# Kernel optimization log

Measured on AMD Instinct MI355X. Metric: run time of the kernel, lower is better.

Reference implementation:

```python
import jax, jax.numpy as jnp
import numpy as np

D_MODEL = 1024
N_HEADS = 16
HEAD_DIM = D_MODEL // N_HEADS
SPARSITY = 0.5  # torch.rand(...) < sparsity_factor -> True means masked (disallowed)


def setup_inputs() -> dict:
    key = jax.random.key(0)
    ks = jax.random.split(key, 12)
    B, S, D = 2, 2048, D_MODEL
    query = jax.random.normal(ks[0], (B, S, D), dtype=jnp.float32)
    key_t = jax.random.normal(ks[1], (B, S, D), dtype=jnp.float32)
    value = jax.random.normal(ks[2], (B, S, D), dtype=jnp.float32)
    # per-forward random boolean mask, materialized deterministically here
    mask = jax.random.uniform(ks[3], (B, S, S)) < SPARSITY
    scale = 1.0 / np.sqrt(D)
    Wq = jax.random.uniform(ks[4], (D, D), jnp.float32, -scale, scale)
    Wk = jax.random.uniform(ks[5], (D, D), jnp.float32, -scale, scale)
    Wv = jax.random.uniform(ks[6], (D, D), jnp.float32, -scale, scale)
    Wo = jax.random.uniform(ks[7], (D, D), jnp.float32, -scale, scale)
    bq = jnp.zeros((D,), jnp.float32)
    bk = jnp.zeros((D,), jnp.float32)
    bv = jnp.zeros((D,), jnp.float32)
    bo = jnp.zeros((D,), jnp.float32)
    return {"query": query, "key": key_t, "value": value, "mask": mask,
            "Wq": Wq, "Wk": Wk, "Wv": Wv, "Wo": Wo,
            "bq": bq, "bk": bk, "bv": bv, "bo": bo}


def reference(query, key, value, mask, Wq, Wk, Wv, Wo, bq, bk, bv, bo):
    B, S, D = query.shape
    H, hd = N_HEADS, HEAD_DIM
    # in-projections (torch uses x @ W.T + b)
    q = (query @ Wq.T + bq).reshape(B, S, H, hd).transpose(0, 2, 1, 3)  # (B,H,S,hd)
    k = (key @ Wk.T + bk).reshape(B, S, H, hd).transpose(0, 2, 1, 3)
    v = (value @ Wv.T + bv).reshape(B, S, H, hd).transpose(0, 2, 1, 3)
    scores = jnp.einsum('bhqd,bhkd->bhqk', q, k) / jnp.sqrt(jnp.float32(hd))
    # bool mask: True = disallowed; broadcast over heads
    scores = jnp.where(mask[:, None, :, :], -jnp.inf, scores)
    attn = jax.nn.softmax(scores, axis=-1)  # dropout inactive at eval
    out = jnp.einsum('bhqk,bhkd->bhqd', attn, v)  # (B,H,S,hd)
    out = out.transpose(0, 2, 1, 3).reshape(B, S, D)
    return out @ Wo.T + bo
```

## Files before the change

### kernel.cpp

```cpp
#include <hip/hip_runtime.h>
#include <stdint.h>

#define MTOK   4096
#define DMODEL 1024
#define SEQ    2048
#define NH     16
#define HD     64
#define LDK    72
#define LDP    72
#define QSCL   0.18033688f
#define NWORDS (2 * SEQ * SEQ / 64)

typedef _Float16 h8  __attribute__((ext_vector_type(8)));
typedef _Float16 h4  __attribute__((ext_vector_type(4)));
typedef _Float16 h2  __attribute__((ext_vector_type(2)));
typedef __fp16   fp16x2 __attribute__((ext_vector_type(2)));
typedef float    f16v __attribute__((ext_vector_type(16)));
typedef float    f4  __attribute__((ext_vector_type(4)));

typedef __attribute__((address_space(1))) const unsigned int g_u32;
typedef __attribute__((address_space(3))) unsigned int       l_u32;

__device__ __forceinline__ void g2l16(const void* g, void* l) {
    __builtin_amdgcn_global_load_lds((g_u32*)(unsigned long long)g,
                                     (l_u32*)(unsigned int)(unsigned long long)l,
                                     16, 0, 0);
}

__device__ __forceinline__ h2 pkrtz(float a, float b) {
    fp16x2 r = __builtin_amdgcn_cvt_pkrtz(a, b);
    return __builtin_bit_cast(h2, r);
}

#if __has_builtin(__builtin_amdgcn_exp2f)
#define E2(x) __builtin_amdgcn_exp2f(x)
#else
#define E2(x) exp2f(x)
#endif

__global__ __launch_bounds__(256) void prep_kernel(
    const float* __restrict__ s0, const float* __restrict__ s1,
    const float* __restrict__ s2, const float* __restrict__ s3,
    const float* __restrict__ s4, const float* __restrict__ s5,
    const float* __restrict__ s6,
    _Float16* __restrict__ d0, _Float16* __restrict__ d1,
    _Float16* __restrict__ d2, _Float16* __restrict__ d3,
    _Float16* __restrict__ d4, _Float16* __restrict__ d5,
    _Float16* __restrict__ d6,
    const unsigned char* __restrict__ mb, const unsigned int* __restrict__ mu,
    unsigned long long* __restrict__ mout) {
    const int z = blockIdx.y;
    const int gid = blockIdx.x * 256 + threadIdx.x;
    const int stride = gridDim.x * 256;
    if (z < 7) {
        const float* s = (z == 0) ? s0 : (z == 1) ? s1 : (z == 2) ? s2
                       : (z == 3) ? s3 : (z == 4) ? s4 : (z == 5) ? s5 : s6;
        _Float16* d = (z == 0) ? d0 : (z == 1) ? d1 : (z == 2) ? d2
                    : (z == 3) ? d3 : (z == 4) ? d4 : (z == 5) ? d5 : d6;
        const int n4 = (z < 3) ? (MTOK * DMODEL / 4) : (DMODEL * DMODEL / 4);
        for (int i = gid; i < n4; i += stride) {
            float4 v = ((const float4*)s)[i];
            h4 o = {(_Float16)v.x, (_Float16)v.y, (_Float16)v.z, (_Float16)v.w};
            ((h4*)d)[i] = o;
        }
    } else {
        __shared__ int wsum[4];
        int cnt = 0;
        const uchar4* mp4 = (const uchar4*)mb;
#pragma unroll
        for (int i = 0; i < 8; ++i) {
            uchar4 v = mp4[threadIdx.x * 8 + i];
            cnt += (v.x != 0) + (v.y != 0) + (v.z != 0) + (v.w != 0);
        }
#pragma unroll
        for (int off = 32; off > 0; off >>= 1) cnt += __shfl_down(cnt, off, 64);
        if ((threadIdx.x & 63) == 0) wsum[threadIdx.x >> 6] = cnt;
        __syncthreads();
        const int byteflag = (wsum[0] + wsum[1] + wsum[2] + wsum[3]) > 2500;

        for (int w = gid; w < NWORDS; w += stride) {
            unsigned long long bits = 0ull;
            if (byteflag) {
                const uint4* p = (const uint4*)(mb + (size_t)w * 64);
#pragma unroll
                for (int i = 0; i < 4; ++i) {
                    uint4 v = p[i];
                    unsigned dw[4] = {v.x, v.y, v.z, v.w};
#pragma unroll
                    for (int j = 0; j < 4; ++j) {
                        unsigned d = dw[j];
                        unsigned nib = (unsigned)((d & 0xFFu) != 0)
                                     | ((unsigned)((d & 0xFF00u) != 0) << 1)
                                     | ((unsigned)((d & 0xFF0000u) != 0) << 2)
                                     | ((unsigned)((d >> 24) != 0) << 3);
                        bits |= (unsigned long long)nib << (i * 16 + j * 4);
                    }
                }
            } else {
                const uint4* p = (const uint4*)(mu + (size_t)w * 64);
#pragma unroll
                for (int i = 0; i < 16; ++i) {
                    uint4 v = p[i];
                    unsigned nib = (unsigned)(v.x != 0u)
                                 | ((unsigned)(v.y != 0u) << 1)
                                 | ((unsigned)(v.z != 0u) << 2)
                                 | ((unsigned)(v.w != 0u) << 3);
                    bits |= (unsigned long long)nib << (i * 4);
                }
            }
            mout[w] = bits;
        }
    }
}

template <int MODE, int BM, int BN>
__device__ __forceinline__ void gemm16_body(const _Float16* __restrict__ A,
                                            const _Float16* __restrict__ W,
                                            const float* __restrict__ bias,
                                            void* __restrict__ outv,
                                            float scale) {
    __shared__ __align__(16) _Float16 Asb[BM * 64];
    __shared__ __align__(16) _Float16 Bsb[BN * 64];
    constexpr int NI = BM / 32, NJ = BN / 32;
    constexpr int WM = BM / 2,  WN = BN / 2;
    constexpr int RA = BM * 128 / 4096;
    constexpr int RB = BN * 128 / 4096;
    const int tid = threadIdx.x;
    const int wv = tid >> 6, lane = tid & 63;
    const int l15 = lane & 15, g = lane >> 4;
    const int wy = wv >> 1, wx = wv & 1;
    const int m0 = blockIdx.x * BM, n0 = blockIdx.y * BN;

    f4 acc[NI][NJ];
#pragma unroll
    for (int i = 0; i < NI; ++i)
#pragma unroll
        for (int j = 0; j < NJ; ++j) acc[i][j] = (f4){0.f, 0.f, 0.f, 0.f};

    const char* Ab = (const char*)A;
    const char* Wb = (const char*)W;
    int srowA[RA], scolA[RA];
#pragma unroll
    for (int r = 0; r < RA; ++r) {
        const int o = (r * 256 + tid) * 16;
        srowA[r] = o >> 7;
        scolA[r] = (((o >> 4) & 7) ^ (srowA[r] & 7)) * 16;
    }
    int srowB[RB], scolB[RB];
#pragma unroll
    for (int r = 0; r < RB; ++r) {
        const int o = (r * 256 + tid) * 16;
        srowB[r] = o >> 7;
        scolB[r] = (((o >> 4) & 7) ^ (srowB[r] & 7)) * 16;
    }

    for (int kt = 0; kt < 16; ++kt) {
        const int k0b = kt * 128;
        __syncthreads();
#pragma unroll
        for (int r = 0; r < RA; ++r)
            g2l16(Ab + (size_t)(m0 + srowA[r]) * 2048 + k0b + scolA[r],
                  (char*)Asb + (r * 256 + tid) * 16);
#pragma unroll
        for (int r = 0; r < RB; ++r)
            g2l16(Wb + (size_t)(n0 + srowB[r]) * 2048 + k0b + scolB[r],
                  (char*)Bsb + (r * 256 + tid) * 16);
        __syncthreads();

#pragma unroll
        for (int ksub = 0; ksub < 2; ++ksub) {
            h8 af[NI], bf[NJ];
#pragma unroll
            for (int t = 0; t < NI; ++t) {
                const int row = wy * WM + t * 16 + l15;
                const int pos = (ksub * 4 + g) ^ (row & 7);
                af[t] = *(const h8*)(Asb + row * 64 + pos * 8);
            }
#pragma unroll
            for (int t = 0; t < NJ; ++t) {
                const int row = wx * WN + t * 16 + l15;
                const int pos = (ksub * 4 + g) ^ (row & 7);
                bf[t] = *(const h8*)(Bsb + row * 64 + pos * 8);
            }
#pragma unroll
            for (int i = 0; i < NI; ++i)
#pragma unroll
                for (int j = 0; j < NJ; ++j) {
                    if (MODE == 2)
                        acc[i][j] = __builtin_amdgcn_mfma_f32_16x16x32_f16(
                            bf[j], af[i], acc[i][j], 0, 0, 0);
                    else
                        acc[i][j] = __builtin_amdgcn_mfma_f32_16x16x32_f16(
                            af[i], bf[j], acc[i][j], 0, 0, 0);
                }
        }
    }

#pragma unroll
    for (int j = 0; j < NJ; ++j) {
#pragma unroll
        for (int i = 0; i < NI; ++i) {
            if (MODE == 2) {
                const int m = m0 + wy * WM + i * 16 + l15;
                const int b = m >> 11, s = m & 2047;
#pragma unroll
                for (int r = 0; r < 4; ++r) {
                    const int n = n0 + wx * WN + j * 16 + g * 4 + r;
                    const int h = n >> 6, d = n & 63;
                    ((_Float16*)outv)[(((size_t)(b * NH + h)) * HD + d) * SEQ + s] =
                        (_Float16)(acc[i][j][r] + bias[n]);
                }
            } else {
                const int n = n0 + wx * WN + j * 16 + l15;
                const float bb = bias[n];
                const int mbase = m0 + wy * WM + i * 16 + g * 4;
                if (MODE == 1) {
                    const int h = n >> 6, d = n & 63;
#pragma unroll
                    for (int r = 0; r < 4; ++r) {
                        const int m = mbase + r;
                        const int b = m >> 11, s = m & 2047;
                        ((_Float16*)outv)[(((size_t)(b * NH + h)) * SEQ + s) * HD + d] =
                            (_Float16)((acc[i][j][r] + bb) * scale);
                    }
                } else {
#pragma unroll
                    for (int r = 0; r < 4; ++r)
                        ((float*)outv)[(size_t)(mbase + r) * DMODEL + n] =
                            acc[i][j][r] + bb;
                }
            }
        }
    }
}

__global__ __launch_bounds__(256) void qkv_gemm16_kernel(
    const _Float16* __restrict__ xq, const _Float16* __restrict__ xk,
    const _Float16* __restrict__ xv,
    const _Float16* __restrict__ Wq, const _Float16* __restrict__ Wk,
    const _Float16* __restrict__ Wv,
    const float* __restrict__ bq, const float* __restrict__ bk,
    const float* __restrict__ bv,
    _Float16* __restrict__ q_out, _Float16* __restrict__ k_out,
    _Float16* __restrict__ vt_out) {
    const int z = blockIdx.z;
    if (z == 0)      gemm16_body<1, 128, 128>(xq, Wq, bq, (void*)q_out, QSCL);
    else if (z == 1) gemm16_body<1, 128, 128>(xk, Wk, bk, (void*)k_out, 1.0f);
    else             gemm16_body<2, 128, 128>(xv, Wv, bv, (void*)vt_out, 1.0f);
}

__global__ __launch_bounds__(256) void out_gemm16_kernel(
    const _Float16* __restrict__ X, const _Float16* __restrict__ W,
    const float* __restrict__ bias, float* __restrict__ out) {
    gemm16_body<0, 64, 128>(X, W, bias, (void*)out, 1.0f);
}

__global__ __launch_bounds__(256) void attn_kernel(
    const _Float16* __restrict__ Q, const _Float16* __restrict__ K,
    const _Float16* __restrict__ Vt,
    const unsigned long long* __restrict__ mbits,
    _Float16* __restrict__ out) {
    __shared__ __align__(16) _Float16 Ks[2][64 * LDK];
    __shared__ __align__(16) _Float16 Vs[2][64 * LDK];
    __shared__ __align__(16) _Float16 Ps[128 * LDP];

    const int tid = threadIdx.x;
    const int wv = tid >> 6, lane = tid & 63;
    const int l31 = lane & 31, hi = lane >> 5;
    const int q0 = blockIdx.x * 128;
    const int bh = blockIdx.y;
    const int b = bh >> 4, h = bh & 15;
    const size_t bho = (size_t)bh * (SEQ * HD);
    const int qrow = q0 + wv * 32 + l31;

    h8 qf[4];
    const _Float16* qp = Q + bho + (size_t)qrow * HD;
#pragma unroll
    for (int ks = 0; ks < 4; ++ks) qf[ks] = *(const h8*)(qp + ks * 16 + hi * 8);

    f16v Ot[2];
#pragma unroll
    for (int mt = 0; mt < 2; ++mt)
#pragma unroll
        for (int r = 0; r < 16; ++r) Ot[mt][r] = 0.f;
    float l_r = 0.f;

    const int sr = tid >> 2;
    const int scol = (tid & 3) * 16;
    const _Float16* kg = K + bho;
    const _Float16* vg = Vt + bho;
    _Float16* prow = &Ps[(wv * 32 + l31) * LDP];
    const unsigned long long* mrow =
        mbits + ((size_t)b * SEQ + qrow) * (SEQ / 64);

    h8 kr0 = *(const h8*)(kg + (size_t)sr * HD + scol);
    h8 kr1 = *(const h8*)(kg + (size_t)sr * HD + scol + 8);
    h8 vr0 = *(const h8*)(vg + (size_t)sr * SEQ + scol);
    h8 vr1 = *(const h8*)(vg + (size_t)sr * SEQ + scol + 8);
    uint2 mw = *(const uint2*)(mrow);
    *(h8*)(&Ks[0][sr * LDK + scol])     = kr0;
    *(h8*)(&Ks[0][sr * LDK + scol + 8]) = kr1;
    *(h8*)(&Vs[0][sr * LDK + scol])     = vr0;
    *(h8*)(&Vs[0][sr * LDK + scol + 8]) = vr1;
    __syncthreads();

    for (int kt = 0; kt < 32; ++kt) {
        const int cur = kt & 1;
        uint2 mw_n;
        if (kt < 31) {
            const int k0n = (kt + 1) * 64;
            kr0 = *(const h8*)(kg + (size_t)(k0n + sr) * HD + scol);
            kr1 = *(const h8*)(kg + (size_t)(k0n + sr) * HD + scol + 8);
            vr0 = *(const h8*)(vg + (size_t)sr * SEQ + k0n + scol);
            vr1 = *(const h8*)(vg + (size_t)sr * SEQ + k0n + scol + 8);
            mw_n = *(const uint2*)(mrow + kt + 1);
        }

        f16v sc0, sc1;
#pragma unroll
        for (int r = 0; r < 16; ++r) { sc0[r] = 0.f; sc1[r] = 0.f; }
#pragma unroll
        for (int ks = 0; ks < 4; ++ks) {
            h8 kf0 = *(const h8*)(&Ks[cur][l31 * LDK + ks * 16 + hi * 8]);
            h8 kf1 = *(const h8*)(&Ks[cur][(32 + l31) * LDK + ks * 16 + hi * 8]);
            sc0 = __builtin_amdgcn_mfma_f32_32x32x16_f16(kf0, qf[ks], sc0, 0, 0, 0);
            sc1 = __builtin_amdgcn_mfma_f32_32x32x16_f16(kf1, qf[ks], sc1, 0, 0, 0);
        }

        float ps = 0.f;
#pragma unroll
        for (int mt = 0; mt < 2; ++mt) {
            const unsigned w = mt ? mw.y : mw.x;
            const f16v& s = mt ? sc1 : sc0;
#pragma unroll
            for (int g4 = 0; g4 < 4; ++g4) {
                const int sh = g4 * 8 + hi * 4;
                float p0 = E2(((w >> (sh + 0)) & 1u) ? -1e30f : s[g4 * 4 + 0]);
                float p1 = E2(((w >> (sh + 1)) & 1u) ? -1e30f : s[g4 * 4 + 1]);
                float p2 = E2(((w >> (sh + 2)) & 1u) ? -1e30f : s[g4 * 4 + 2]);
                float p3 = E2(((w >> (sh + 3)) & 1u) ? -1e30f : s[g4 * 4 + 3]);
                h2 lo  = pkrtz(p0, p1);
                h2 hi2 = pkrtz(p2, p3);
                ps += p0 + p1 + p2 + p3;
                h4 ph = {lo.x, lo.y, hi2.x, hi2.y};
                *(h4*)(prow + mt * 32 + g4 * 8 + hi * 4) = ph;
            }
        }
        l_r += ps;

        h8 pf[4];
#pragma unroll
        for (int ks = 0; ks < 4; ++ks)
            pf[ks] = *(const h8*)(prow + ks * 16 + hi * 8);
#pragma unroll
        for (int ks = 0; ks < 4; ++ks) {
            h8 vf0 = *(const h8*)(&Vs[cur][l31 * LDK + ks * 16 + hi * 8]);
            h8 vf1 = *(const h8*)(&Vs[cur][(32 + l31) * LDK + ks * 16 + hi * 8]);
            Ot[0] = __builtin_amdgcn_mfma_f32_32x32x16_f16(vf0, pf[ks], Ot[0], 0, 0, 0);
            Ot[1] = __builtin_amdgcn_mfma_f32_32x32x16_f16(vf1, pf[ks], Ot[1], 0, 0, 0);
        }

        if (kt < 31) {
            const int nxt = cur ^ 1;
            *(h8*)(&Ks[nxt][sr * LDK + scol])     = kr0;
            *(h8*)(&Ks[nxt][sr * LDK + scol + 8]) = kr1;
            *(h8*)(&Vs[nxt][sr * LDK + scol])     = vr0;
            *(h8*)(&Vs[nxt][sr * LDK + scol + 8]) = vr1;
            mw = mw_n;
        }
        __syncthreads();
    }

    l_r += __shfl_xor(l_r, 32);
    const float inv = 1.0f / l_r;
    _Float16* op = out + ((size_t)b * SEQ + qrow) * DMODEL + h * HD;
#pragma unroll
    for (int mt = 0; mt < 2; ++mt)
#pragma unroll
        for (int g4 = 0; g4 < 4; ++g4) {
            const int d = mt * 32 + g4 * 8 + hi * 4;
            h4 ov = {(_Float16)(Ot[mt][g4 * 4 + 0] * inv),
                     (_Float16)(Ot[mt][g4 * 4 + 1] * inv),
                     (_Float16)(Ot[mt][g4 * 4 + 2] * inv),
                     (_Float16)(Ot[mt][g4 * 4 + 3] * inv)};
            *(h4*)(op + d) = ov;
        }
}

extern "C" void kernel_launch(void* const* d_in, const int* in_sizes, int n_in,
                              void* d_out, int out_size, void* d_ws, size_t ws_size,
                              hipStream_t stream) {
    const float* query = (const float*)d_in[0];
    const float* key_  = (const float*)d_in[1];
    const float* value = (const float*)d_in[2];
    const void*  mask  = d_in[3];
    const float* Wq = (const float*)d_in[4];
    const float* Wk = (const float*)d_in[5];
    const float* Wv = (const float*)d_in[6];
    const float* Wo = (const float*)d_in[7];
    const float* bq = (const float*)d_in[8];
    const float* bk = (const float*)d_in[9];
    const float* bv = (const float*)d_in[10];
    const float* bo = (const float*)d_in[11];

    char* ws = (char*)d_ws;
    _Float16* xq  = (_Float16*)(ws + 256);
    _Float16* xk  = xq + (size_t)MTOK * DMODEL;
    _Float16* xv  = xk + (size_t)MTOK * DMODEL;
    _Float16* Wqh = xv + (size_t)MTOK * DMODEL;
    _Float16* Wkh = Wqh + (size_t)DMODEL * DMODEL;
    _Float16* Wvh = Wkh + (size_t)DMODEL * DMODEL;
    _Float16* Woh = Wvh + (size_t)DMODEL * DMODEL;
    _Float16* q_ws  = Woh + (size_t)DMODEL * DMODEL;
    _Float16* k_ws  = q_ws + (size_t)MTOK * DMODEL;
    _Float16* vt_ws = k_ws + (size_t)MTOK * DMODEL;
    _Float16* a_ws  = vt_ws + (size_t)MTOK * DMODEL;
    unsigned long long* mb_ws =
        (unsigned long long*)(a_ws + (size_t)MTOK * DMODEL);

    prep_kernel<<<dim3(1024, 8), 256, 0, stream>>>(
        query, key_, value, Wq, Wk, Wv, Wo, xq, xk, xv, Wqh, Wkh, Wvh, Woh,
        (const unsigned char*)mask, (const unsigned int*)mask, mb_ws);

    dim3 gqkv(MTOK / 128, DMODEL / 128, 3);
    qkv_gemm16_kernel<<<gqkv, 256, 0, stream>>>(xq, xk, xv, Wqh, Wkh, Wvh,
                                                bq, bk, bv, q_ws, k_ws, vt_ws);

    dim3 gattn(SEQ / 128, 2 * NH);
    attn_kernel<<<gattn, 256, 0, stream>>>(q_ws, k_ws, vt_ws, mb_ws, a_ws);

    dim3 gout(MTOK / 64, DMODEL / 128);
    out_gemm16_kernel<<<gout, 256, 0, stream>>>(a_ws, Woh, bo, (float*)d_out);
}
```

Measured before the change: 276.0 us.

## Split attention KV loop across two wave groups and keep P in registers

The attention kernel now uses 512 threads, and two groups of four waves each process alternate 64-key tiles for the same 128 queries. Their partial outputs and row sums are merged through shared memory at the end. The P matrix no longer goes through an LDS round-trip: v_permlane32_swap rearranges the packed fp16 probabilities in registers into MFMA operand layout, and row sums are taken with fdot2 on the rounded values. s_setprio is raised around the MFMA blocks. This buys more parallelism per CU and less LDS traffic, at the cost of a final merge step and more LDS per block.

```diff
diff --git a/kernel.cpp b/kernel.cpp
--- a/kernel.cpp
+++ b/kernel.cpp
@@ -7,7 +7,6 @@
 #define NH     16
 #define HD     64
 #define LDK    72
-#define LDP    72
 #define QSCL   0.18033688f
 #define NWORDS (2 * SEQ * SEQ / 64)
 
@@ -17,6 +16,7 @@
 typedef __fp16   fp16x2 __attribute__((ext_vector_type(2)));
 typedef float    f16v __attribute__((ext_vector_type(16)));
 typedef float    f4  __attribute__((ext_vector_type(4)));
+typedef int      iv4 __attribute__((ext_vector_type(4)));
 
 typedef __attribute__((address_space(1))) const unsigned int g_u32;
 typedef __attribute__((address_space(3))) unsigned int       l_u32;
@@ -37,6 +37,16 @@
 #else
 #define E2(x) exp2f(x)
 #endif
+
+__device__ __forceinline__ float dot2sum(int v, float acc) {
+    h2 a = __builtin_bit_cast(h2, v);
+#if __has_builtin(__builtin_amdgcn_fdot2)
+    h2 one2 = {(_Float16)1.0f, (_Float16)1.0f};
+    return __builtin_amdgcn_fdot2(a, one2, acc, false);
+#else
+    return acc + (float)a.x + (float)a.y;
+#endif
+}
 
 __global__ __launch_bounds__(256) void prep_kernel(
     const float* __restrict__ s0, const float* __restrict__ s1,
@@ -255,23 +265,23 @@
     gemm16_body<0, 64, 128>(X, W, bias, (void*)out, 1.0f);
 }
 
-__global__ __launch_bounds__(256) void attn_kernel(
+__global__ __launch_bounds__(512, 4) void attn_kernel(
     const _Float16* __restrict__ Q, const _Float16* __restrict__ K,
     const _Float16* __restrict__ Vt,
     const unsigned long long* __restrict__ mbits,
     _Float16* __restrict__ out) {
-    __shared__ __align__(16) _Float16 Ks[2][64 * LDK];
-    __shared__ __align__(16) _Float16 Vs[2][64 * LDK];
-    __shared__ __align__(16) _Float16 Ps[128 * LDP];
+    __shared__ __align__(16) _Float16 Ks[2][2][64 * LDK];
+    __shared__ __align__(16) _Float16 Vs[2][2][64 * LDK];
 
     const int tid = threadIdx.x;
     const int wv = tid >> 6, lane = tid & 63;
+    const int grp = wv >> 2, wvg = wv & 3;
     const int l31 = lane & 31, hi = lane >> 5;
     const int q0 = blockIdx.x * 128;
     const int bh = blockIdx.y;
     const int b = bh >> 4, h = bh & 15;
     const size_t bho = (size_t)bh * (SEQ * HD);
-    const int qrow = q0 + wv * 32 + l31;
+    const int qrow = q0 + wvg * 32 + l31;
 
     h8 qf[4];
     const _Float16* qp = Q + bho + (size_t)qrow * HD;
@@ -285,106 +295,136 @@
         for (int r = 0; r < 16; ++r) Ot[mt][r] = 0.f;
     float l_r = 0.f;
 
-    const int sr = tid >> 2;
-    const int scol = (tid & 3) * 16;
+    const int gtid = tid & 255;
+    const int sr = gtid >> 2;
+    const int scol = (gtid & 3) * 16;
     const _Float16* kg = K + bho;
     const _Float16* vg = Vt + bho;
-    _Float16* prow = &Ps[(wv * 32 + l31) * LDP];
     const unsigned long long* mrow =
         mbits + ((size_t)b * SEQ + qrow) * (SEQ / 64);
 
-    h8 kr0 = *(const h8*)(kg + (size_t)sr * HD + scol);
-    h8 kr1 = *(const h8*)(kg + (size_t)sr * HD + scol + 8);
-    h8 vr0 = *(const h8*)(vg + (size_t)sr * SEQ + scol);
-    h8 vr1 = *(const h8*)(vg + (size_t)sr * SEQ + scol + 8);
-    uint2 mw = *(const uint2*)(mrow);
-    *(h8*)(&Ks[0][sr * LDK + scol])     = kr0;
-    *(h8*)(&Ks[0][sr * LDK + scol + 8]) = kr1;
-    *(h8*)(&Vs[0][sr * LDK + scol])     = vr0;
-    *(h8*)(&Vs[0][sr * LDK + scol + 8]) = vr1;
+    {
+        const int k0 = grp * 64;
+        h8 a0 = *(const h8*)(kg + (size_t)(k0 + sr) * HD + scol);
+        h8 a1 = *(const h8*)(kg + (size_t)(k0 + sr) * HD + scol + 8);
+        h8 a2 = *(const h8*)(vg + (size_t)sr * SEQ + k0 + scol);
+        h8 a3 = *(const h8*)(vg + (size_t)sr * SEQ + k0 + scol + 8);
+        *(h8*)(&Ks[grp][0][sr * LDK + scol])     = a0;
+        *(h8*)(&Ks[grp][0][sr * LDK + scol + 8]) = a1;
+        *(h8*)(&Vs[grp][0][sr * LDK + scol])     = a2;
+        *(h8*)(&Vs[grp][0][sr * LDK + scol + 8]) = a3;
+    }
+    uint2 mw = *(const uint2*)(mrow + grp);
     __syncthreads();
 
-    for (int kt = 0; kt < 32; ++kt) {
-        const int cur = kt & 1;
+    for (int it = 0; it < 16; ++it) {
+        const int cur = it & 1;
+        const int kt = 2 * it + grp;
+        h8 kr0, kr1, vr0, vr1;
         uint2 mw_n;
-        if (kt < 31) {
-            const int k0n = (kt + 1) * 64;
+        if (it < 15) {
+            const int k0n = (kt + 2) * 64;
             kr0 = *(const h8*)(kg + (size_t)(k0n + sr) * HD + scol);
             kr1 = *(const h8*)(kg + (size_t)(k0n + sr) * HD + scol + 8);
             vr0 = *(const h8*)(vg + (size_t)sr * SEQ + k0n + scol);
             vr1 = *(const h8*)(vg + (size_t)sr * SEQ + k0n + scol + 8);
-            mw_n = *(const uint2*)(mrow + kt + 1);
+            mw_n = *(const uint2*)(mrow + kt + 2);
         }
 
         f16v sc0, sc1;
 #pragma unroll
         for (int r = 0; r < 16; ++r) { sc0[r] = 0.f; sc1[r] = 0.f; }
+        __builtin_amdgcn_s_setprio(1);
 #pragma unroll
         for (int ks = 0; ks < 4; ++ks) {
-            h8 kf0 = *(const h8*)(&Ks[cur][l31 * LDK + ks * 16 + hi * 8]);
-            h8 kf1 = *(const h8*)(&Ks[cur][(32 + l31) * LDK + ks * 16 + hi * 8]);
+            h8 kf0 = *(const h8*)(&Ks[grp][cur][l31 * LDK + ks * 16 + hi * 8]);
+            h8 kf1 = *(const h8*)(&Ks[grp][cur][(32 + l31) * LDK + ks * 16 + hi * 8]);
             sc0 = __builtin_amdgcn_mfma_f32_32x32x16_f16(kf0, qf[ks], sc0, 0, 0, 0);
             sc1 = __builtin_amdgcn_mfma_f32_32x32x16_f16(kf1, qf[ks], sc1, 0, 0, 0);
         }
-
-        float ps = 0.f;
+        __builtin_amdgcn_s_setprio(0);
+
+        int rp[8][2];
 #pragma unroll
         for (int mt = 0; mt < 2; ++mt) {
             const unsigned w = mt ? mw.y : mw.x;
+            const unsigned wl = w >> (hi * 4);
             const f16v& s = mt ? sc1 : sc0;
 #pragma unroll
             for (int g4 = 0; g4 < 4; ++g4) {
-                const int sh = g4 * 8 + hi * 4;
-                float p0 = E2(((w >> (sh + 0)) & 1u) ? -1e30f : s[g4 * 4 + 0]);
-                float p1 = E2(((w >> (sh + 1)) & 1u) ? -1e30f : s[g4 * 4 + 1]);
-                float p2 = E2(((w >> (sh + 2)) & 1u) ? -1e30f : s[g4 * 4 + 2]);
-                float p3 = E2(((w >> (sh + 3)) & 1u) ? -1e30f : s[g4 * 4 + 3]);
-                h2 lo  = pkrtz(p0, p1);
-                h2 hi2 = pkrtz(p2, p3);
-                ps += p0 + p1 + p2 + p3;
-                h4 ph = {lo.x, lo.y, hi2.x, hi2.y};
-                *(h4*)(prow + mt * 32 + g4 * 8 + hi * 4) = ph;
-            }
-        }
-        l_r += ps;
-
-        h8 pf[4];
-#pragma unroll
-        for (int ks = 0; ks < 4; ++ks)
-            pf[ks] = *(const h8*)(prow + ks * 16 + hi * 8);
+                float p0 = E2(((wl >> (g4 * 8 + 0)) & 1u) ? -1e30f : s[g4 * 4 + 0]);
+                float p1 = E2(((wl >> (g4 * 8 + 1)) & 1u) ? -1e30f : s[g4 * 4 + 1]);
+                float p2 = E2(((wl >> (g4 * 8 + 2)) & 1u) ? -1e30f : s[g4 * 4 + 2]);
+                float p3 = E2(((wl >> (g4 * 8 + 3)) & 1u) ? -1e30f : s[g4 * 4 + 3]);
+                rp[mt * 4 + g4][0] = __builtin_bit_cast(int, pkrtz(p0, p1));
+                rp[mt * 4 + g4][1] = __builtin_bit_cast(int, pkrtz(p2, p3));
+            }
+        }
+
+        float l0 = 0.f, l1 = 0.f;
 #pragma unroll
         for (int ks = 0; ks < 4; ++ks) {
-            h8 vf0 = *(const h8*)(&Vs[cur][l31 * LDK + ks * 16 + hi * 8]);
-            h8 vf1 = *(const h8*)(&Vs[cur][(32 + l31) * LDK + ks * 16 + hi * 8]);
-            Ot[0] = __builtin_amdgcn_mfma_f32_32x32x16_f16(vf0, pf[ks], Ot[0], 0, 0, 0);
-            Ot[1] = __builtin_amdgcn_mfma_f32_32x32x16_f16(vf1, pf[ks], Ot[1], 0, 0, 0);
-        }
-
-        if (kt < 31) {
+            int a0 = rp[2 * ks][0], a1 = rp[2 * ks][1];
+            int b0 = rp[2 * ks + 1][0], b1 = rp[2 * ks + 1][1];
+            asm volatile("v_permlane32_swap_b32 %0, %1" : "+v"(a0), "+v"(b0));
+            asm volatile("v_permlane32_swap_b32 %0, %1" : "+v"(a1), "+v"(b1));
+            l0 = dot2sum(a0, l0); l1 = dot2sum(a1, l1);
+            l0 = dot2sum(b0, l0); l1 = dot2sum(b1, l1);
+            iv4 pi = {a0, a1, b0, b1};
+            h8 pf = __builtin_bit_cast(h8, pi);
+            __builtin_amdgcn_s_setprio(1);
+            h8 vf0 = *(const h8*)(&Vs[grp][cur][l31 * LDK + ks * 16 + hi * 8]);
+            h8 vf1 = *(const h8*)(&Vs[grp][cur][(32 + l31) * LDK + ks * 16 + hi * 8]);
+            Ot[0] = __builtin_amdgcn_mfma_f32_32x32x16_f16(vf0, pf, Ot[0], 0, 0, 0);
+            Ot[1] = __builtin_amdgcn_mfma_f32_32x32x16_f16(vf1, pf, Ot[1], 0, 0, 0);
+            __builtin_amdgcn_s_setprio(0);
+        }
+        l_r += l0 + l1;
+
+        if (it < 15) {
             const int nxt = cur ^ 1;
-            *(h8*)(&Ks[nxt][sr * LDK + scol])     = kr0;
-            *(h8*)(&Ks[nxt][sr * LDK + scol + 8]) = kr1;
-            *(h8*)(&Vs[nxt][sr * LDK + scol])     = vr0;
-            *(h8*)(&Vs[nxt][sr * LDK + scol + 8]) = vr1;
+            *(h8*)(&Ks[grp][nxt][sr * LDK + scol])     = kr0;
+            *(h8*)(&Ks[grp][nxt][sr * LDK + scol + 8]) = kr1;
+            *(h8*)(&Vs[grp][nxt][sr * LDK + scol])     = vr0;
+            *(h8*)(&Vs[grp][nxt][sr * LDK + scol + 8]) = vr1;
             mw = mw_n;
         }
         __syncthreads();
     }
 
     l_r += __shfl_xor(l_r, 32);
-    const float inv = 1.0f / l_r;
-    _Float16* op = out + ((size_t)b * SEQ + qrow) * DMODEL + h * HD;
-#pragma unroll
-    for (int mt = 0; mt < 2; ++mt)
-#pragma unroll
-        for (int g4 = 0; g4 < 4; ++g4) {
-            const int d = mt * 32 + g4 * 8 + hi * 4;
-            h4 ov = {(_Float16)(Ot[mt][g4 * 4 + 0] * inv),
-                     (_Float16)(Ot[mt][g4 * 4 + 1] * inv),
-                     (_Float16)(Ot[mt][g4 * 4 + 2] * inv),
-                     (_Float16)(Ot[mt][g4 * 4 + 3] * inv)};
-            *(h4*)(op + d) = ov;
-        }
+    float* mrg = (float*)&Ks[0][0][0];
+    float* lm  = (float*)&Vs[0][0][0];
+    const int ql = wvg * 32 + l31;
+    if (grp == 1) {
+#pragma unroll
+        for (int mt = 0; mt < 2; ++mt)
+#pragma unroll
+            for (int t = 0; t < 4; ++t) {
+                f4 v = {Ot[mt][t * 4 + 0], Ot[mt][t * 4 + 1],
+                        Ot[mt][t * 4 + 2], Ot[mt][t * 4 + 3]};
+                *(f4*)&mrg[ql * 64 + mt * 32 + t * 8 + hi * 4] = v;
+            }
+        if (hi == 0) lm[ql] = l_r;
+    }
+    __syncthreads();
+    if (grp == 0) {
+        l_r += lm[ql];
+        const float inv = 1.0f / l_r;
+        _Float16* op = out + ((size_t)b * SEQ + qrow) * DMODEL + h * HD;
+#pragma unroll
+        for (int mt = 0; mt < 2; ++mt)
+#pragma unroll
+            for (int t = 0; t < 4; ++t) {
+                const int d = mt * 32 + t * 8 + hi * 4;
+                f4 v = *(const f4*)&mrg[ql * 64 + d];
+                h4 ov = {(_Float16)((Ot[mt][t * 4 + 0] + v.x) * inv),
+                         (_Float16)((Ot[mt][t * 4 + 1] + v.y) * inv),
+                         (_Float16)((Ot[mt][t * 4 + 2] + v.z) * inv),
+                         (_Float16)((Ot[mt][t * 4 + 3] + v.w) * inv)};
+                *(h4*)(op + d) = ov;
+            }
+    }
 }
 
 extern "C" void kernel_launch(void* const* d_in, const int* in_sizes, int n_in,
@@ -427,7 +467,7 @@
                                                 bq, bk, bv, q_ws, k_ws, vt_ws);
 
     dim3 gattn(SEQ / 128, 2 * NH);
-    attn_kernel<<<gattn, 256, 0, stream>>>(q_ws, k_ws, vt_ws, mb_ws, a_ws);
+    attn_kernel<<<gattn, 512, 0, stream>>>(q_ws, k_ws, vt_ws, mb_ws, a_ws);
 
     dim3 gout(MTOK / 64, DMODEL / 128);
     out_gemm16_kernel<<<gout, 256, 0, stream>>>(a_ws, Woh, bo, (float*)d_out);
```

After: 269.6 us. 1.02x faster.
